# Performance work log

Measured on AMD Instinct MI355X. Metric: run time of the kernel, lower is better.

## Reference

```python
import jax, jax.numpy as jnp
import numpy as np

EPS_LN = 1e-5


def fwht(x):
    """Fast Walsh-Hadamard transform over the last axis (power-of-two length).
    Vectorized butterfly: log2(n) stages, each a reshape + add/sub."""
    orig_shape = x.shape
    n = orig_shape[-1]
    y = x.reshape(-1, n)
    h = 1
    while h < n:
        y = y.reshape(-1, n // (2 * h), 2, h)
        a = y[:, :, 0, :]
        b = y[:, :, 1, :]
        y = jnp.stack([a + b, a - b], axis=2).reshape(-1, n)
        h <<= 1
    return y.reshape(orig_shape)


def setup_inputs() -> dict:
    key = jax.random.key(0)
    kx, kw, kg = jax.random.split(key, 3)
    B, S, D_IN, D_OUT = 4, 4096, 2048, 2048
    x = jax.random.normal(kx, (B, S, D_IN), dtype=jnp.float32)
    # kaiming_uniform_(a=sqrt(5)) -> bound = 1/sqrt(in_features)
    bound = 1.0 / np.sqrt(D_IN)
    W = jax.random.uniform(kw, (D_OUT, D_IN), dtype=jnp.float32,
                           minval=-bound, maxval=bound)
    gamma = jnp.ones((D_IN,), dtype=jnp.float32)
    beta = jnp.zeros((D_IN,), dtype=jnp.float32)
    return {"x": x, "W": W, "gamma": gamma, "beta": beta}


def reference(x, W, gamma, beta):
    bits = 4
    max_val = (1 << (bits - 1)) - 1  # 7
    # LayerNorm over last dim
    mu = jnp.mean(x, axis=-1, keepdims=True)
    var = jnp.mean(jnp.square(x - mu), axis=-1, keepdims=True)
    x_ln = (x - mu) * jax.lax.rsqrt(var + EPS_LN) * gamma + beta
    # Activation fake-quant to `bits` bits (per-row absmax scale)
    x_scale = jnp.clip(jnp.max(jnp.abs(x_ln), axis=-1, keepdims=True), 1e-6, None)
    x_int = jnp.clip(jnp.round(x_ln * max_val / x_scale), -max_val, max_val)
    x_q = x_int * x_scale / max_val
    # Hadamard transform of quantized activations
    x_h = fwht(x_q)
    # Ternary weight quantization with global mean-abs scale
    w_scale = jnp.clip(jnp.mean(jnp.abs(W)), 1e-6, None)
    w_q = (jnp.where(W > 0.5 * w_scale, 1.0, 0.0)
           + jnp.where(W < -0.5 * w_scale, -1.0, 0.0)) * w_scale
    # Linear (no bias), then second Hadamard transform
    out = jnp.einsum('bsd,od->bso', x_h, w_q)
    return fwht(out)
```

## Files before the change

### kernel.cpp

```cpp
#include <hip/hip_runtime.h>

typedef unsigned short u16;
typedef __attribute__((ext_vector_type(8))) __bf16 bf16x8;
typedef __attribute__((ext_vector_type(4))) float floatx4;

#define DDIM 2048
#define MROWS 16384

__device__ __forceinline__ u16 f2bf(float f) {
    unsigned int u = __builtin_bit_cast(unsigned int, f);
    u = (u + 0x7fffu + ((u >> 16) & 1u)) >> 16;
    return (u16)u;
}

__device__ __forceinline__ float wave_sum(float v) {
#pragma unroll
    for (int o = 32; o > 0; o >>= 1) v += __shfl_down(v, o, 64);
    return v;
}
__device__ __forceinline__ float wave_max(float v) {
#pragma unroll
    for (int o = 32; o > 0; o >>= 1) v = fmaxf(v, __shfl_down(v, o, 64));
    return v;
}

__global__ __launch_bounds__(256) void absmean_part(const float4* __restrict__ W4,
                                                    float* __restrict__ partial) {
    float s = 0.f;
    for (int i = blockIdx.x * 256 + threadIdx.x; i < (DDIM * DDIM / 4); i += 1024 * 256) {
        float4 v = W4[i];
        s += fabsf(v.x) + fabsf(v.y) + fabsf(v.z) + fabsf(v.w);
    }
    s = wave_sum(s);
    __shared__ float red[4];
    if ((threadIdx.x & 63) == 0) red[threadIdx.x >> 6] = s;
    __syncthreads();
    if (threadIdx.x == 0) partial[blockIdx.x] = red[0] + red[1] + red[2] + red[3];
}

template <bool QUANT>
__global__ __launch_bounds__(256) void transpose_k(const float* __restrict__ in,
                                                   float* __restrict__ out,
                                                   const float* __restrict__ partial) {
    __shared__ float tile[64][65];
    const int t = threadIdx.x;
    float wsc = 0.f, half_t = 0.f;
    if (QUANT) {
        __shared__ float wred[4];
        float s = partial[t] + partial[t + 256] + partial[t + 512] + partial[t + 768];
        s = wave_sum(s);
        if ((t & 63) == 0) wred[t >> 6] = s;
        __syncthreads();
        float m = (wred[0] + wred[1] + wred[2] + wred[3]) * (1.0f / (float)(DDIM * DDIM));
        wsc = fmaxf(m, 1e-6f);
        half_t = 0.5f * wsc;
        __syncthreads();
    }
    const int tx = t & 63;
    const int ty = t >> 6;
    const int r0 = blockIdx.y * 64;
    const int c0 = blockIdx.x * 64;
#pragma unroll
    for (int i = 0; i < 16; ++i) {
        int r = ty + i * 4;
        float w = in[(size_t)(r0 + r) * DDIM + c0 + tx];
        if (QUANT) w = (w > half_t ? wsc : 0.f) + (w < -half_t ? -wsc : 0.f);
        tile[r][tx] = w;
    }
    __syncthreads();
#pragma unroll
    for (int i = 0; i < 16; ++i) {
        int r = ty + i * 4;
        out[(size_t)(c0 + r) * DDIM + r0 + tx] = tile[tx][r];
    }
}

template <bool BF16OUT>
__global__ __launch_bounds__(256) void fwht_rows(const float* __restrict__ in,
                                                 void* __restrict__ out) {
    __shared__ float s0[DDIM];
    __shared__ float s1[DDIM];
    const int row = blockIdx.x;
    const int t = threadIdx.x;
    const int lane = t & 63;
    const float4* rp = (const float4*)(in + (size_t)row * DDIM);
    float4 a = rp[t], b = rp[t + 256];
    float v[8] = {a.x, a.y, a.z, a.w, b.x, b.y, b.z, b.w};

#pragma unroll
    for (int h = 1; h <= 4; h <<= 1)
#pragma unroll
        for (int j = 0; j < 8; ++j)
            if (!(j & h)) { float x = v[j], y = v[j | h]; v[j] = x + y; v[j | h] = x - y; }

#pragma unroll
    for (int m = 1; m <= 32; m <<= 1)
#pragma unroll
        for (int j = 0; j < 8; ++j) {
            float p = __shfl_xor(v[j], m, 64);
            v[j] = (lane & m) ? (p - v[j]) : (p + v[j]);
        }

    ((float4*)s0)[2 * t] = make_float4(v[0], v[1], v[2], v[3]);
    ((float4*)s0)[2 * t + 1] = make_float4(v[4], v[5], v[6], v[7]);
    __syncthreads();
    {
        int p1 = t ^ 64;
        float4 pa = ((const float4*)s0)[2 * p1], pb = ((const float4*)s0)[2 * p1 + 1];
        float pv[8] = {pa.x, pa.y, pa.z, pa.w, pb.x, pb.y, pb.z, pb.w};
#pragma unroll
        for (int j = 0; j < 8; ++j) v[j] = (t & 64) ? (pv[j] - v[j]) : (pv[j] + v[j]);
    }
    ((float4*)s1)[2 * t] = make_float4(v[0], v[1], v[2], v[3]);
    ((float4*)s1)[2 * t + 1] = make_float4(v[4], v[5], v[6], v[7]);
    __syncthreads();
    {
        int p2 = t ^ 128;
        float4 pa = ((const float4*)s1)[2 * p2], pb = ((const float4*)s1)[2 * p2 + 1];
        float pv[8] = {pa.x, pa.y, pa.z, pa.w, pb.x, pb.y, pb.z, pb.w};
#pragma unroll
        for (int j = 0; j < 8; ++j) v[j] = (t & 128) ? (pv[j] - v[j]) : (pv[j] + v[j]);
    }

    if (BF16OUT) {
        u16* op = (u16*)out + (size_t)row * DDIM;
        uint2 o0, o1;
        o0.x = (unsigned)f2bf(v[0]) | ((unsigned)f2bf(v[1]) << 16);
        o0.y = (unsigned)f2bf(v[2]) | ((unsigned)f2bf(v[3]) << 16);
        o1.x = (unsigned)f2bf(v[4]) | ((unsigned)f2bf(v[5]) << 16);
        o1.y = (unsigned)f2bf(v[6]) | ((unsigned)f2bf(v[7]) << 16);
        ((uint2*)op)[t] = o0;
        ((uint2*)op)[t + 256] = o1;
    } else {
        float* op = (float*)out + (size_t)row * DDIM;
        ((float4*)op)[t] = make_float4(v[0], v[1], v[2], v[3]);
        ((float4*)op)[t + 256] = make_float4(v[4], v[5], v[6], v[7]);
    }
}

__global__ __launch_bounds__(256) void ln_quant(const float* __restrict__ X,
                                                const float* __restrict__ G,
                                                const float* __restrict__ Bt,
                                                u16* __restrict__ XQ) {
    const int row = blockIdx.x;
    const int t = threadIdx.x;
    const float4* rp = (const float4*)(X + (size_t)row * DDIM);
    float4 v0 = rp[t], v1 = rp[t + 256];
    float v[8] = {v0.x, v0.y, v0.z, v0.w, v1.x, v1.y, v1.z, v1.w};

    __shared__ float redA[4], redB[4], redC[4];
    const int wv = t >> 6, ln = t & 63;

    float s = 0.f, s2 = 0.f;
#pragma unroll
    for (int j = 0; j < 8; ++j) { s += v[j]; s2 += v[j] * v[j]; }
#pragma unroll
    for (int o = 32; o > 0; o >>= 1) {
        s += __shfl_down(s, o, 64);
        s2 += __shfl_down(s2, o, 64);
    }
    if (ln == 0) { redA[wv] = s; redB[wv] = s2; }
    __syncthreads();
    const float mu = (redA[0] + redA[1] + redA[2] + redA[3]) * (1.f / (float)DDIM);
    const float ex2 = (redB[0] + redB[1] + redB[2] + redB[3]) * (1.f / (float)DDIM);
    const float var = ex2 - mu * mu;
    const float rstd = rsqrtf(var + 1e-5f);

    const float4* gp = (const float4*)G;
    const float4* bp = (const float4*)Bt;
    float4 g0 = gp[t], g1 = gp[t + 256];
    float4 b0 = bp[t], b1 = bp[t + 256];
    float gg[8] = {g0.x, g0.y, g0.z, g0.w, g1.x, g1.y, g1.z, g1.w};
    float bb[8] = {b0.x, b0.y, b0.z, b0.w, b1.x, b1.y, b1.z, b1.w};

    float y[8];
    float am = 0.f;
#pragma unroll
    for (int j = 0; j < 8; ++j) {
        y[j] = (v[j] - mu) * rstd * gg[j] + bb[j];
        am = fmaxf(am, fabsf(y[j]));
    }
    float w = wave_max(am);
    if (ln == 0) redC[wv] = w;
    __syncthreads();
    const float scale = fmaxf(fmaxf(fmaxf(redC[0], redC[1]), fmaxf(redC[2], redC[3])), 1e-6f);

    const float r7 = 7.f / scale, s7 = scale / 7.f;
    unsigned int q[4];
#pragma unroll
    for (int j = 0; j < 8; j += 2) {
        float qa = fminf(fmaxf(rintf(y[j] * r7), -7.f), 7.f);
        float qb = fminf(fmaxf(rintf(y[j + 1] * r7), -7.f), 7.f);
        q[j >> 1] = (unsigned)f2bf(qa * s7) | ((unsigned)f2bf(qb * s7) << 16);
    }
    uint2 o0, o1;
    o0.x = q[0]; o0.y = q[1]; o1.x = q[2]; o1.y = q[3];
    uint2* orow = (uint2*)(XQ + (size_t)row * DDIM);
    orow[t] = o0;
    orow[t + 256] = o1;
}

#define GBK 64
#define GNT (DDIM / GBK)
#define NITER (GNT / 2)
#define TILEU (256 * GBK)

__device__ __forceinline__ void gl_lds16(const u16* g, u16* l) {
    __builtin_amdgcn_global_load_lds((const __attribute__((address_space(1))) void*)g,
                                     (__attribute__((address_space(3))) void*)l,
                                     16, 0, 0);
}

#define PBAR do {                                                              \
    __builtin_amdgcn_sched_barrier(0);                                         \
    asm volatile("" ::: "memory");                                             \
    __builtin_amdgcn_s_barrier();                                              \
    asm volatile("" ::: "memory");                                             \
    __builtin_amdgcn_sched_barrier(0);                                         \
} while (0)

#define PWAIT8 do {                                                            \
    __builtin_amdgcn_sched_barrier(0);                                         \
    asm volatile("s_waitcnt vmcnt(8)" ::: "memory");                           \
    __builtin_amdgcn_s_barrier();                                              \
    asm volatile("" ::: "memory");                                             \
    __builtin_amdgcn_sched_barrier(0);                                         \
} while (0)

#define PWAIT0 do {                                                            \
    __builtin_amdgcn_sched_barrier(0);                                         \
    asm volatile("s_waitcnt vmcnt(0)" ::: "memory");                           \
    __builtin_amdgcn_s_barrier();                                              \
    asm volatile("" ::: "memory");                                             \
    __builtin_amdgcn_sched_barrier(0);                                         \
} while (0)

__global__ __launch_bounds__(512, 2) void gemm256(const u16* __restrict__ A,
                                                  const u16* __restrict__ B,
                                                  float* __restrict__ C) {
    extern __shared__ __align__(16) u16 lds[];
    const int t = threadIdx.x;
    const int lane = t & 63;
    const int wid = t >> 6;
    const int wm = wid >> 2;
    const int wn = wid & 3;

    const int d = blockIdx.x;
    const int bm = (d & 7) | ((d >> 6) << 3);
    const int bn = (d >> 3) & 7;

    const int l15 = lane & 15;
    const int kq = lane >> 4;
    const int x7 = lane & 7;
    const int c0 = (kq ^ x7) << 3;
    const int c1 = ((kq | 4) ^ x7) << 3;
    const int arow = (wm << 7) + l15;
    const int brow = (wn << 6) + l15;

    const int srow = t >> 3;
    const int gch = ((t & 7) ^ (srow & 7)) << 3;
    const u16* Ag = A + (size_t)(bm * 256 + srow) * DDIM + gch;
    const u16* Bg = B + (size_t)(bn * 256 + srow) * DDIM + gch;
    u16* const AL0 = lds + t * 8;
    u16* const BL0 = lds + TILEU + t * 8;
    u16* const AL1 = lds + 2 * TILEU + t * 8;
    u16* const BL1 = lds + 3 * TILEU + t * 8;
    const u16* const Ab0 = lds;
    const u16* const Bb0 = lds + TILEU;
    const u16* const Ab1 = lds + 2 * TILEU;
    const u16* const Bb1 = lds + 3 * TILEU;

    floatx4 acc[8][4];
#pragma unroll
    for (int i = 0; i < 8; ++i)
#pragma unroll
        for (int j = 0; j < 4; ++j)
#pragma unroll
            for (int e = 0; e < 4; ++e) acc[i][j][e] = 0.f;

    bf16x8 a[4][2], b0v[2][2], b1v[2][2];

#define STGA(dst, q, ko) gl_lds16(Ag + (size_t)((q) * 64) * DDIM + (ko), (dst) + (q) * 4096)
#define STGB(dst, q, ko) gl_lds16(Bg + (size_t)((q) * 64) * DDIM + (ko), (dst) + (q) * 4096)

#define LDA(Ab, mh)                                                            \
    _Pragma("unroll") for (int fm = 0; fm < 4; ++fm) {                         \
        const u16* p = (Ab) + (arow + (mh) * 64 + fm * 16) * GBK;              \
        a[fm][0] = *(const bf16x8*)(p + c0);                                   \
        a[fm][1] = *(const bf16x8*)(p + c1);                                   \
    }

#define LDB(dst, Bb, nh)                                                       \
    _Pragma("unroll") for (int fn = 0; fn < 2; ++fn) {                         \
        const u16* p = (Bb) + (brow + (nh) * 32 + fn * 16) * GBK;              \
        dst[fn][0] = *(const bf16x8*)(p + c0);                                 \
        dst[fn][1] = *(const bf16x8*)(p + c1);                                 \
    }

#define MMA(mh, bsrc, nh)                                                      \
    __builtin_amdgcn_s_setprio(1);                                             \
    _Pragma("unroll") for (int fm = 0; fm < 4; ++fm)                           \
        _Pragma("unroll") for (int fn = 0; fn < 2; ++fn)                       \
            _Pragma("unroll") for (int ks = 0; ks < 2; ++ks)                   \
                acc[(mh) * 4 + fm][(nh) * 2 + fn] =                            \
                    __builtin_amdgcn_mfma_f32_16x16x32_bf16(                   \
                        a[fm][ks], bsrc[fn][ks],                               \
                        acc[(mh) * 4 + fm][(nh) * 2 + fn], 0, 0, 0);           \
    __builtin_amdgcn_s_setprio(0);

#pragma unroll
    for (int q = 0; q < 4; ++q) STGA(AL0, q, 0);
#pragma unroll
    for (int q = 0; q < 4; ++q) STGB(BL0, q, 0);
#pragma unroll
    for (int q = 0; q < 4; ++q) STGA(AL1, q, GBK);
#pragma unroll
    for (int q = 0; q < 4; ++q) STGB(BL1, q, GBK);
    PWAIT8;

    for (int it = 0; it < NITER; ++it) {
        const int kp0 = (it * 2 + 2) * GBK;
        const int kp1 = kp0 + GBK;
        const bool pf = (it < NITER - 1);

        LDA(Ab0, 0);
        LDB(b0v, Bb0, 0);
        PBAR;
        MMA(0, b0v, 0);
        LDB(b1v, Bb0, 1);
        if (pf) { STGA(AL0, 0, kp0); STGA(AL0, 2, kp0); }
        PBAR;
        MMA(0, b1v, 1);
        LDA(Ab0, 1);
        if (pf) { STGB(BL0, 0, kp0); STGB(BL0, 1, kp0); }
        PBAR;
        MMA(1, b0v, 0);
        if (pf) { STGB(BL0, 2, kp0); STGB(BL0, 3, kp0); STGA(AL0, 1, kp0); STGA(AL0, 3, kp0); }
        if (pf) { PWAIT8; } else { PWAIT0; }
        MMA(1, b1v, 1);

        LDA(Ab1, 0);
        LDB(b0v, Bb1, 0);
        PBAR;
        MMA(0, b0v, 0);
        LDB(b1v, Bb1, 1);
        if (pf) { STGA(AL1, 0, kp1); STGA(AL1, 2, kp1); }
        PBAR;
        MMA(0, b1v, 1);
        LDA(Ab1, 1);
        if (pf) { STGB(BL1, 0, kp1); STGB(BL1, 1, kp1); }
        PBAR;
        MMA(1, b0v, 0);
        if (pf) { STGB(BL1, 2, kp1); STGB(BL1, 3, kp1); STGA(AL1, 1, kp1); STGA(AL1, 3, kp1); }
        if (pf) { PWAIT8; } else { PWAIT0; }
        MMA(1, b1v, 1);
    }

#undef STGA
#undef STGB
#undef LDA
#undef LDB
#undef MMA

    float* Cb = C + (size_t)(bm * 256 + (wm << 7) + (lane >> 4) * 4) * DDIM
                  + bn * 256 + (wn << 6) + l15;
#pragma unroll
    for (int fm = 0; fm < 8; ++fm)
#pragma unroll
        for (int fn = 0; fn < 4; ++fn)
#pragma unroll
            for (int r = 0; r < 4; ++r)
                Cb[(size_t)(fm * 16 + r) * DDIM + fn * 16] = acc[fm][fn][r];
}

extern "C" void kernel_launch(void* const* d_in, const int* in_sizes, int n_in,
                              void* d_out, int out_size, void* d_ws, size_t ws_size,
                              hipStream_t stream) {
    const float* X  = (const float*)d_in[0];
    const float* W  = (const float*)d_in[1];
    const float* G  = (const float*)d_in[2];
    const float* Bt = (const float*)d_in[3];
    float* out = (float*)d_out;

    char* ws = (char*)d_ws;
    u16*   xq   = (u16*)ws;
    float* bufA = (float*)(ws + (size_t)67108864);
    float* bufB = (float*)(ws + (size_t)67108864 + 16777216);
    float* partial = bufB;
    u16*   w3      = (u16*)bufB;

    absmean_part<<<1024, 256, 0, stream>>>((const float4*)W, partial);
    transpose_k<true><<<dim3(32, 32), 256, 0, stream>>>(W, bufA, partial);
    fwht_rows<false><<<2048, 256, 0, stream>>>(bufA, (void*)bufB);
    transpose_k<false><<<dim3(32, 32), 256, 0, stream>>>(bufB, bufA, nullptr);
    fwht_rows<true><<<2048, 256, 0, stream>>>(bufA, (void*)w3);
    ln_quant<<<MROWS, 256, 0, stream>>>(X, G, Bt, xq);
    hipFuncSetAttribute(reinterpret_cast<const void*>(gemm256),
                        hipFuncAttributeMaxDynamicSharedMemorySize, 131072);
    gemm256<<<dim3(512), 512, 131072, stream>>>(xq, w3, out);
}
```

Before: 377.0 us.

## Restructure GEMM main loop with pre/post barriers and explicit LDS waitcnt pacing

Replaces the single barrier before each MFMA cluster with a pre-barrier that also waits on LDS counters and a post-barrier after each MFMA cluster, bracketing compute phases in a ping-pong style. Adds an lgkmcnt(8) pacing wait after the first LDS reads, and moves one B-tile global-to-LDS stage earlier to rebalance prefetch issue across the phases. The aim is better interleaving of LDS reads, global prefetch and MFMA across the two co-resident blocks. The extra barriers per iteration add synchronisation cost and could stall waves.

```diff
diff --git a/kernel.cpp b/kernel.cpp
--- a/kernel.cpp
+++ b/kernel.cpp
@@ -211,29 +211,29 @@
                                      16, 0, 0);
 }
 
-#define PBAR do {                                                              \
-    __builtin_amdgcn_sched_barrier(0);                                         \
-    asm volatile("" ::: "memory");                                             \
+#define PRE do {                                                               \
+    __builtin_amdgcn_sched_barrier(0);                                         \
     __builtin_amdgcn_s_barrier();                                              \
-    asm volatile("" ::: "memory");                                             \
+    asm volatile("s_waitcnt lgkmcnt(0)" ::: "memory");                         \
     __builtin_amdgcn_sched_barrier(0);                                         \
 } while (0)
 
-#define PWAIT8 do {                                                            \
-    __builtin_amdgcn_sched_barrier(0);                                         \
-    asm volatile("s_waitcnt vmcnt(8)" ::: "memory");                           \
+#define PREVM(pf) do {                                                         \
+    __builtin_amdgcn_sched_barrier(0);                                         \
+    if (pf) asm volatile("s_waitcnt vmcnt(8)" ::: "memory");                   \
+    else    asm volatile("s_waitcnt vmcnt(0)" ::: "memory");                   \
     __builtin_amdgcn_s_barrier();                                              \
-    asm volatile("" ::: "memory");                                             \
+    asm volatile("s_waitcnt lgkmcnt(0)" ::: "memory");                         \
     __builtin_amdgcn_sched_barrier(0);                                         \
 } while (0)
 
-#define PWAIT0 do {                                                            \
-    __builtin_amdgcn_sched_barrier(0);                                         \
-    asm volatile("s_waitcnt vmcnt(0)" ::: "memory");                           \
+#define POST do {                                                              \
+    __builtin_amdgcn_sched_barrier(0);                                         \
     __builtin_amdgcn_s_barrier();                                              \
-    asm volatile("" ::: "memory");                                             \
     __builtin_amdgcn_sched_barrier(0);                                         \
 } while (0)
+
+#define PACE12 asm volatile("s_waitcnt lgkmcnt(8)" ::: "memory")
 
 __global__ __launch_bounds__(512, 2) void gemm256(const u16* __restrict__ A,
                                                   const u16* __restrict__ B,
@@ -316,7 +316,10 @@
     for (int q = 0; q < 4; ++q) STGA(AL1, q, GBK);
 #pragma unroll
     for (int q = 0; q < 4; ++q) STGB(BL1, q, GBK);
-    PWAIT8;
+    __builtin_amdgcn_sched_barrier(0);
+    asm volatile("s_waitcnt vmcnt(8)" ::: "memory");
+    __builtin_amdgcn_s_barrier();
+    __builtin_amdgcn_sched_barrier(0);
 
     for (int it = 0; it < NITER; ++it) {
         const int kp0 = (it * 2 + 2) * GBK;
@@ -325,35 +328,45 @@
 
         LDA(Ab0, 0);
         LDB(b0v, Bb0, 0);
-        PBAR;
+        PACE12;
+        PRE;
         MMA(0, b0v, 0);
+        POST;
         LDB(b1v, Bb0, 1);
         if (pf) { STGA(AL0, 0, kp0); STGA(AL0, 2, kp0); }
-        PBAR;
+        PRE;
         MMA(0, b1v, 1);
+        POST;
         LDA(Ab0, 1);
-        if (pf) { STGB(BL0, 0, kp0); STGB(BL0, 1, kp0); }
-        PBAR;
+        if (pf) { STGB(BL0, 0, kp0); STGB(BL0, 1, kp0); STGB(BL0, 2, kp0); }
+        PRE;
         MMA(1, b0v, 0);
-        if (pf) { STGB(BL0, 2, kp0); STGB(BL0, 3, kp0); STGA(AL0, 1, kp0); STGA(AL0, 3, kp0); }
-        if (pf) { PWAIT8; } else { PWAIT0; }
+        POST;
+        if (pf) { STGB(BL0, 3, kp0); STGA(AL0, 1, kp0); STGA(AL0, 3, kp0); }
+        PREVM(pf);
         MMA(1, b1v, 1);
+        POST;
 
         LDA(Ab1, 0);
         LDB(b0v, Bb1, 0);
-        PBAR;
+        PACE12;
+        PRE;
         MMA(0, b0v, 0);
+        POST;
         LDB(b1v, Bb1, 1);
         if (pf) { STGA(AL1, 0, kp1); STGA(AL1, 2, kp1); }
-        PBAR;
+        PRE;
         MMA(0, b1v, 1);
+        POST;
         LDA(Ab1, 1);
-        if (pf) { STGB(BL1, 0, kp1); STGB(BL1, 1, kp1); }
-        PBAR;
+        if (pf) { STGB(BL1, 0, kp1); STGB(BL1, 1, kp1); STGB(BL1, 2, kp1); }
+        PRE;
         MMA(1, b0v, 0);
-        if (pf) { STGB(BL1, 2, kp1); STGB(BL1, 3, kp1); STGA(AL1, 1, kp1); STGA(AL1, 3, kp1); }
-        if (pf) { PWAIT8; } else { PWAIT0; }
+        POST;
+        if (pf) { STGB(BL1, 3, kp1); STGA(AL1, 1, kp1); STGA(AL1, 3, kp1); }
+        PREVM(pf);
         MMA(1, b1v, 1);
+        POST;
     }
 
 #undef STGA
```

After: 386.2 us. +2.4%, slower.

## Fuse weight transpose and row FWHT into column-wise FWHT kernel

Applied to the files above, without the earlier changes.

Replaces the four-kernel weight preprocessing chain (transpose+quant, row FWHT, transpose, row FWHT) with two kernels. Each loads an 8-column strip of the full 2048-row matrix into LDS, runs the Hadamard butterflies down the columns in shared memory with radix-4 stages, and writes the result transposed. This removes two launches and two full round-trips of the 16 MB matrix through global memory. In exchange it uses about 73 KB of LDS per block and only 256 blocks, so occupancy drops and the strided column loads may be less efficient.

```diff
diff --git a/kernel.cpp b/kernel.cpp
--- a/kernel.cpp
+++ b/kernel.cpp
@@ -38,12 +38,16 @@
     if (threadIdx.x == 0) partial[blockIdx.x] = red[0] + red[1] + red[2] + red[3];
 }
 
-template <bool QUANT>
-__global__ __launch_bounds__(256) void transpose_k(const float* __restrict__ in,
-                                                   float* __restrict__ out,
-                                                   const float* __restrict__ partial) {
-    __shared__ float tile[64][65];
+#define CFP 9
+
+template <bool QUANT, bool BF16OUT>
+__global__ __launch_bounds__(256) void colfwht(const float* __restrict__ in,
+                                               void* __restrict__ out,
+                                               const float* __restrict__ partial) {
+    extern __shared__ float S[];
     const int t = threadIdx.x;
+    const int c8 = blockIdx.x * 8;
+
     float wsc = 0.f, half_t = 0.f;
     if (QUANT) {
         __shared__ float wred[4];
@@ -54,87 +58,75 @@
         float m = (wred[0] + wred[1] + wred[2] + wred[3]) * (1.0f / (float)(DDIM * DDIM));
         wsc = fmaxf(m, 1e-6f);
         half_t = 0.5f * wsc;
+    }
+
+#pragma unroll
+    for (int i = 0; i < 16; ++i) {
+        const int k = i * 256 + t;
+        const int row = k >> 1, half = k & 1;
+        float4 v = *(const float4*)(in + (size_t)row * DDIM + c8 + half * 4);
+        if (QUANT) {
+            v.x = (v.x > half_t ? wsc : 0.f) + (v.x < -half_t ? -wsc : 0.f);
+            v.y = (v.y > half_t ? wsc : 0.f) + (v.y < -half_t ? -wsc : 0.f);
+            v.z = (v.z > half_t ? wsc : 0.f) + (v.z < -half_t ? -wsc : 0.f);
+            v.w = (v.w > half_t ? wsc : 0.f) + (v.w < -half_t ? -wsc : 0.f);
+        }
+        float* sp = S + row * CFP + half * 4;
+        sp[0] = v.x; sp[1] = v.y; sp[2] = v.z; sp[3] = v.w;
+    }
+    __syncthreads();
+
+#pragma unroll
+    for (int s = 0; s < 5; ++s) {
+        const int h = 1 << (2 * s);
+#pragma unroll
+        for (int i = 0; i < 16; ++i) {
+            const int task = i * 256 + t;
+            const int p = task >> 3, c = task & 7;
+            const int i0 = ((p >> (2 * s)) << (2 * s + 2)) | (p & (h - 1));
+            float* a0 = S + (size_t)i0 * CFP + c;
+            const float x0 = a0[0];
+            const float x1 = a0[(size_t)h * CFP];
+            const float x2 = a0[(size_t)2 * h * CFP];
+            const float x3 = a0[(size_t)3 * h * CFP];
+            const float s01 = x0 + x1, d01 = x0 - x1;
+            const float s23 = x2 + x3, d23 = x2 - x3;
+            a0[0]                   = s01 + s23;
+            a0[(size_t)h * CFP]     = d01 + d23;
+            a0[(size_t)2 * h * CFP] = s01 - s23;
+            a0[(size_t)3 * h * CFP] = d01 - d23;
+        }
         __syncthreads();
     }
-    const int tx = t & 63;
-    const int ty = t >> 6;
-    const int r0 = blockIdx.y * 64;
-    const int c0 = blockIdx.x * 64;
+#pragma unroll
+    for (int i = 0; i < 32; ++i) {
+        const int task = i * 256 + t;
+        const int p = task >> 3, c = task & 7;
+        float* a0 = S + (size_t)p * CFP + c;
+        const float x0 = a0[0];
+        const float x1 = a0[(size_t)1024 * CFP];
+        a0[0] = x0 + x1;
+        a0[(size_t)1024 * CFP] = x0 - x1;
+    }
+    __syncthreads();
+
+    const int c = t >> 5, l = t & 31;
 #pragma unroll
     for (int i = 0; i < 16; ++i) {
-        int r = ty + i * 4;
-        float w = in[(size_t)(r0 + r) * DDIM + c0 + tx];
-        if (QUANT) w = (w > half_t ? wsc : 0.f) + (w < -half_t ? -wsc : 0.f);
-        tile[r][tx] = w;
-    }
-    __syncthreads();
-#pragma unroll
-    for (int i = 0; i < 16; ++i) {
-        int r = ty + i * 4;
-        out[(size_t)(c0 + r) * DDIM + r0 + tx] = tile[tx][r];
-    }
-}
-
-template <bool BF16OUT>
-__global__ __launch_bounds__(256) void fwht_rows(const float* __restrict__ in,
-                                                 void* __restrict__ out) {
-    __shared__ float s0[DDIM];
-    __shared__ float s1[DDIM];
-    const int row = blockIdx.x;
-    const int t = threadIdx.x;
-    const int lane = t & 63;
-    const float4* rp = (const float4*)(in + (size_t)row * DDIM);
-    float4 a = rp[t], b = rp[t + 256];
-    float v[8] = {a.x, a.y, a.z, a.w, b.x, b.y, b.z, b.w};
-
-#pragma unroll
-    for (int h = 1; h <= 4; h <<= 1)
-#pragma unroll
-        for (int j = 0; j < 8; ++j)
-            if (!(j & h)) { float x = v[j], y = v[j | h]; v[j] = x + y; v[j | h] = x - y; }
-
-#pragma unroll
-    for (int m = 1; m <= 32; m <<= 1)
-#pragma unroll
-        for (int j = 0; j < 8; ++j) {
-            float p = __shfl_xor(v[j], m, 64);
-            v[j] = (lane & m) ? (p - v[j]) : (p + v[j]);
+        const int o4 = i * 32 + l;
+        const float r0 = S[(size_t)(o4 * 4 + 0) * CFP + c];
+        const float r1 = S[(size_t)(o4 * 4 + 1) * CFP + c];
+        const float r2 = S[(size_t)(o4 * 4 + 2) * CFP + c];
+        const float r3 = S[(size_t)(o4 * 4 + 3) * CFP + c];
+        if (BF16OUT) {
+            uint2 v;
+            v.x = (unsigned)f2bf(r0) | ((unsigned)f2bf(r1) << 16);
+            v.y = (unsigned)f2bf(r2) | ((unsigned)f2bf(r3) << 16);
+            ((uint2*)((u16*)out + (size_t)(c8 + c) * DDIM))[o4] = v;
+        } else {
+            ((float4*)((float*)out + (size_t)(c8 + c) * DDIM))[o4] =
+                make_float4(r0, r1, r2, r3);
         }
-
-    ((float4*)s0)[2 * t] = make_float4(v[0], v[1], v[2], v[3]);
-    ((float4*)s0)[2 * t + 1] = make_float4(v[4], v[5], v[6], v[7]);
-    __syncthreads();
-    {
-        int p1 = t ^ 64;
-        float4 pa = ((const float4*)s0)[2 * p1], pb = ((const float4*)s0)[2 * p1 + 1];
-        float pv[8] = {pa.x, pa.y, pa.z, pa.w, pb.x, pb.y, pb.z, pb.w};
-#pragma unroll
-        for (int j = 0; j < 8; ++j) v[j] = (t & 64) ? (pv[j] - v[j]) : (pv[j] + v[j]);
-    }
-    ((float4*)s1)[2 * t] = make_float4(v[0], v[1], v[2], v[3]);
-    ((float4*)s1)[2 * t + 1] = make_float4(v[4], v[5], v[6], v[7]);
-    __syncthreads();
-    {
-        int p2 = t ^ 128;
-        float4 pa = ((const float4*)s1)[2 * p2], pb = ((const float4*)s1)[2 * p2 + 1];
-        float pv[8] = {pa.x, pa.y, pa.z, pa.w, pb.x, pb.y, pb.z, pb.w};
-#pragma unroll
-        for (int j = 0; j < 8; ++j) v[j] = (t & 128) ? (pv[j] - v[j]) : (pv[j] + v[j]);
-    }
-
-    if (BF16OUT) {
-        u16* op = (u16*)out + (size_t)row * DDIM;
-        uint2 o0, o1;
-        o0.x = (unsigned)f2bf(v[0]) | ((unsigned)f2bf(v[1]) << 16);
-        o0.y = (unsigned)f2bf(v[2]) | ((unsigned)f2bf(v[3]) << 16);
-        o1.x = (unsigned)f2bf(v[4]) | ((unsigned)f2bf(v[5]) << 16);
-        o1.y = (unsigned)f2bf(v[6]) | ((unsigned)f2bf(v[7]) << 16);
-        ((uint2*)op)[t] = o0;
-        ((uint2*)op)[t + 256] = o1;
-    } else {
-        float* op = (float*)out + (size_t)row * DDIM;
-        ((float4*)op)[t] = make_float4(v[0], v[1], v[2], v[3]);
-        ((float4*)op)[t + 256] = make_float4(v[4], v[5], v[6], v[7]);
     }
 }
 
@@ -390,11 +382,20 @@
     u16*   w3      = (u16*)bufB;
 
     absmean_part<<<1024, 256, 0, stream>>>((const float4*)W, partial);
-    transpose_k<true><<<dim3(32, 32), 256, 0, stream>>>(W, bufA, partial);
-    fwht_rows<false><<<2048, 256, 0, stream>>>(bufA, (void*)bufB);
-    transpose_k<false><<<dim3(32, 32), 256, 0, stream>>>(bufB, bufA, nullptr);
-    fwht_rows<true><<<2048, 256, 0, stream>>>(bufA, (void*)w3);
+
+    {
+        void (*k1)(const float*, void*, const float*) = colfwht<true, false>;
+        void (*k2)(const float*, void*, const float*) = colfwht<false, true>;
+        hipFuncSetAttribute(reinterpret_cast<const void*>(k1),
+                            hipFuncAttributeMaxDynamicSharedMemorySize, DDIM * CFP * 4);
+        hipFuncSetAttribute(reinterpret_cast<const void*>(k2),
+                            hipFuncAttributeMaxDynamicSharedMemorySize, DDIM * CFP * 4);
+        colfwht<true, false><<<256, 256, DDIM * CFP * 4, stream>>>(W, (void*)bufA, partial);
+        colfwht<false, true><<<256, 256, DDIM * CFP * 4, stream>>>(bufA, (void*)w3, nullptr);
+    }
+
     ln_quant<<<MROWS, 256, 0, stream>>>(X, G, Bt, xq);
+
     hipFuncSetAttribute(reinterpret_cast<const void*>(gemm256),
                         hipFuncAttributeMaxDynamicSharedMemorySize, 131072);
     gemm256<<<dim3(512), 512, 131072, stream>>>(xq, w3, out);
```

Measured after the change: 386.9 us. 2.6% more time.
